# Kernel tuning notes

Hardware: AMD Instinct MI355X
Metric: run time of the kernel (lower is better)

The kernel has to match this reference:

```python
import jax, jax.numpy as jnp
import numpy as np

B, H, W, C = 8, 64, 64, 256
C8 = C // 8  # query/key channels


def setup_inputs() -> dict:
    key = jax.random.key(0)
    ks = jax.random.split(key, 8)
    s = 0.02  # init scale for weights
    return {
        "x": jax.random.normal(ks[0], (B, H, W, C), dtype=jnp.float32),
        "Wq": jax.random.normal(ks[1], (C, C8), dtype=jnp.float32) * s,
        "bq": jnp.zeros((C8,), dtype=jnp.float32),
        "Wk": jax.random.normal(ks[2], (C, C8), dtype=jnp.float32) * s,
        "bk": jnp.zeros((C8,), dtype=jnp.float32),
        "Wv": jax.random.normal(ks[3], (C, C), dtype=jnp.float32) * s,
        "bv": jnp.zeros((C,), dtype=jnp.float32),
        "gamma": jnp.full((1,), 0.5, dtype=jnp.float32),
    }


def reference(x, Wq, bq, Wk, bk, Wv, bv, gamma):
    Bn, Hn, Wn, Cn = x.shape
    N = Hn * Wn
    xf = x.reshape(Bn, N, Cn)            # flatten spatial dims: [B, N, C]
    # 1x1 convs == per-pixel dense projections over channels
    q = xf @ Wq + bq                     # [B, N, C//8]
    k = xf @ Wk + bk                     # [B, N, C//8]
    v = xf @ Wv + bv                     # [B, N, C]
    # energy[b,i,j] = k_i . q_j  (matches tf.matmul(key, query, transpose_b=True))
    energy = jnp.einsum('bic,bjc->bij', k, q)   # [B, N, N]
    attn = jax.nn.softmax(energy, axis=-1)      # softmax over last axis
    # out_i = sum_j attn[i,j] * v_j  (intended SAGAN aggregation in NHWC layout)
    out = jnp.einsum('bij,bjc->bic', attn, v)   # [B, N, C]
    out = out.reshape(Bn, Hn, Wn, Cn)
    return gamma * out + x
```

## Files before the change

kernel.cpp:

```cpp
#include <hip/hip_runtime.h>

typedef __attribute__((ext_vector_type(8))) short short8;
typedef __attribute__((ext_vector_type(4))) float f32x4;
typedef __attribute__((ext_vector_type(16))) float f32x16;
typedef __attribute__((ext_vector_type(2))) unsigned int u32x2;
typedef __attribute__((ext_vector_type(4))) unsigned int u32x4;
typedef unsigned short u16;
typedef unsigned int u32;

#define MFMA16(a, b, c) __builtin_amdgcn_mfma_f32_16x16x32_bf16((a), (b), (c), 0, 0, 0)
#define MFMA32(a, b, c) __builtin_amdgcn_mfma_f32_32x32x16_bf16((a), (b), (c), 0, 0, 0)

#define BAR_VMEM() asm volatile("s_waitcnt vmcnt(0) lgkmcnt(0)\ns_barrier" ::: "memory")
#define BAR_LDS()  asm volatile("s_waitcnt lgkmcnt(0)\ns_barrier" ::: "memory")

#define BATCH 8
#define NTOK 4096
#define CDIM 256
#define CQK 32
#define LOG2E 1.4426950408889634f

__device__ __forceinline__ u16 f2bf(float f) {
  u32 u = __float_as_uint(f);
  return (u16)((u + 0x7FFFu + ((u >> 16) & 1u)) >> 16);
}
__device__ __forceinline__ u32 pack2(float a, float b) {
  const u32 ua = __float_as_uint(a) + 0x8000u;
  const u32 ub = __float_as_uint(b) + 0x8000u;
#if __has_builtin(__builtin_amdgcn_perm)
  return __builtin_amdgcn_perm(ub, ua, 0x07060302u);
#else
  return (ua >> 16) | (ub & 0xFFFF0000u);
#endif
}
__device__ __forceinline__ float fexp2(float x) {
#if __has_builtin(__builtin_amdgcn_exp2f)
  return __builtin_amdgcn_exp2f(x);
#else
  return exp2f(x);
#endif
}
__device__ __forceinline__ void gl_lds16(const u16* g, u16* l) {
  __builtin_amdgcn_global_load_lds(
      (const __attribute__((address_space(1))) unsigned int*)(g),
      (__attribute__((address_space(3))) unsigned int*)(l), 16, 0, 0);
}

__global__ void k_prep(const float* __restrict__ Wq, const float* __restrict__ bq,
                       const float* __restrict__ Wk, const float* __restrict__ bk,
                       const float* __restrict__ Wv, const float* __restrict__ bv,
                       u16* __restrict__ wtf, float* __restrict__ bias) {
  const int f = blockIdx.x;
  const int L = threadIdx.x;
  const int ct = f >> 3, ks = f & 7;
  const int o = ct * 16 + (L & 15);
  const int ch = ks * 32 + (L >> 4) * 8;
  short8 v8;
#pragma unroll
  for (int jj = 0; jj < 8; jj++) {
    const int c = ch + jj;
    float v;
    if (o < 32)       v = Wq[c * CQK + o];
    else if (o < 64)  v = Wk[c * CQK + (o - 32)];
    else              v = Wv[c * CDIM + (o - 64)];
    v8[jj] = (short)f2bf(v);
  }
  *(short8*)(wtf + (size_t)f * 512 + L * 8) = v8;
  if (f == 0) {
    for (int i = L; i < 320; i += 64) {
      if (i < 32)      bias[i] = bq[i];
      else if (i < 64) bias[i] = bk[i - 32];
      else             bias[i] = bv[i - 64];
    }
  }
}

__global__ __launch_bounds__(256, 2) void k_proj(
    const float* __restrict__ x, const u16* __restrict__ wtf,
    const float* __restrict__ bias,
    u16* __restrict__ q_ws, u16* __restrict__ k_ws, u16* __restrict__ vt_ws) {
  __shared__ u16 x_lds[64 * 264];
  __shared__ u16 vt_t[64 * 72];
  const int m0 = blockIdx.x * 64;
  const int tid = threadIdx.x;
  const int w = tid >> 6, L = tid & 63;
  const int lr = L & 15, q4 = L >> 4;

  short8 wfA[5], wfB[5];
#pragma unroll
  for (int j = 0; j < 5; j++)
    wfA[j] = *(const short8*)(wtf + ((size_t)((j * 4 + w) * 8 + 0)) * 512 + L * 8);

#pragma unroll
  for (int ii = 0; ii < 8; ii++) {
    const int e = (tid + 256 * ii) * 8;
    const int row = e >> 8, col = e & 255;
    const float* src = x + (size_t)(m0 + row) * CDIM + col;
    f32x4 a = *(const f32x4*)src;
    f32x4 b4 = *(const f32x4*)(src + 4);
    u32x4 pk;
    pk[0] = pack2(a[0], a[1]);
    pk[1] = pack2(a[2], a[3]);
    pk[2] = pack2(b4[0], b4[1]);
    pk[3] = pack2(b4[2], b4[3]);
    *(u32x4*)&x_lds[row * 264 + col] = pk;
  }
  __syncthreads();

  f32x4 acc[4][5];
#pragma unroll
  for (int rg = 0; rg < 4; rg++)
#pragma unroll
    for (int j = 0; j < 5; j++) acc[rg][j] = (f32x4){0.f, 0.f, 0.f, 0.f};

#pragma unroll
  for (int ks = 0; ks < 8; ks++) {
    if (ks < 7) {
#pragma unroll
      for (int j = 0; j < 5; j++) {
        short8 v = *(const short8*)(wtf +
            ((size_t)((j * 4 + w) * 8 + ks + 1)) * 512 + L * 8);
        if (ks & 1) wfA[j] = v; else wfB[j] = v;
      }
    }
#pragma unroll
    for (int rg = 0; rg < 4; rg++) {
      short8 a = *(const short8*)&x_lds[(rg * 16 + lr) * 264 + ks * 32 + q4 * 8];
#pragma unroll
      for (int j = 0; j < 5; j++)
        acc[rg][j] = MFMA16(a, (ks & 1) ? wfB[j] : wfA[j], acc[rg][j]);
    }
  }

  {
    const float bb = bias[w * 16 + lr];
#pragma unroll
    for (int rg = 0; rg < 4; rg++)
#pragma unroll
      for (int r = 0; r < 4; r++) {
        const int row = m0 + rg * 16 + q4 * 4 + r;
        float v = acc[rg][0][r] + bb;
        if (w < 2) q_ws[(size_t)row * CQK + w * 16 + lr] = f2bf(v);
        else       k_ws[(size_t)row * CQK + (w - 2) * 16 + lr] = f2bf(v * LOG2E);
      }
  }
  const int b = m0 >> 12, nloc = m0 & 4095;
  const int rb2 = ((lr >> 3) & 1) << 2;
  const int c_l = w * 16 + lr;
#pragma unroll
  for (int cg = 0; cg < 4; cg++) {
    __syncthreads();
    const int j = cg + 1;
    const float bb = bias[(4 + cg * 4 + w) * 16 + lr];
#pragma unroll
    for (int rg = 0; rg < 4; rg++) {
      const int n_base = (rg * 16 + q4 * 4) ^ rb2;
      u32x2 pk;
      pk[0] = pack2(acc[rg][j][0] + bb, acc[rg][j][1] + bb);
      pk[1] = pack2(acc[rg][j][2] + bb, acc[rg][j][3] + bb);
      *(u32x2*)&vt_t[c_l * 72 + n_base] = pk;
    }
    __syncthreads();
#pragma unroll
    for (int i = 0; i < 2; i++) {
      const int gch = tid + 256 * i;
      const int cl2 = gch >> 3, jc = gch & 7;
      short8 v = *(const short8*)&vt_t[cl2 * 72 + jc * 8];
      *(short8*)(vt_ws + ((size_t)(b * CDIM + cg * 64 + cl2)) * NTOK + nloc + jc * 8) = v;
    }
  }
}

__global__ __launch_bounds__(256, 2) void k_attn(
    const float* __restrict__ x, const u16* __restrict__ q_ws,
    const u16* __restrict__ k_ws, const u16* __restrict__ vt_ws,
    const float* __restrict__ gamma, float* __restrict__ out) {
  __shared__ u16 vt_lds[2][256 * 64];
  __shared__ u16 p_lds[2][64 * 64];

  const int bid = blockIdx.x;
  const int b = bid & 7;
  const int it = bid >> 3;
  const int i0 = it * 64;
  const int tid = threadIdx.x;
  const int w = tid >> 6, L = tid & 63;
  const int lr = L & 15, q4 = L >> 4;
  const int L31 = L & 31, Lhi = L >> 5, L7 = L & 7;

  const short8 a_k = *(const short8*)(k_ws +
      ((size_t)(b * NTOK + i0 + w * 16 + lr)) * CQK + q4 * 8);

  const int cl_base = tid >> 3;
  const int jc_sw = (tid & 7) ^ (cl_base & 7);
  const u16* vt_g = vt_ws + ((size_t)(b * CDIM + cl_base)) * NTOK + jc_sw * 8;
  const u16* q_base = q_ws + (size_t)b * NTOK * CQK;

  f32x16 o_acc[2][2];
#pragma unroll
  for (int ih = 0; ih < 2; ih++)
#pragma unroll
    for (int ct2 = 0; ct2 < 2; ct2++)
#pragma unroll
      for (int e = 0; e < 16; e++) o_acc[ih][ct2][e] = 0.f;
  float lsum = 0.f;

  const int pw_off = (w * 16 + lr) * 64 + (((q4 & 1) ^ ((lr >> 3) & 1)) << 2);
  const int q4h = q4 >> 1;
  u16* const pl0 = &p_lds[0][0];
  u16* const pl1 = &p_lds[1][0];

#define EXPW(SV, T, PW)                                                          \
  do {                                                                           \
    const float p0 = fexp2((SV)[0]);                                             \
    const float p1 = fexp2((SV)[1]);                                             \
    const float p2 = fexp2((SV)[2]);                                             \
    const float p3 = fexp2((SV)[3]);                                             \
    lsum += (p0 + p1) + (p2 + p3);                                               \
    u32x2 pk;                                                                    \
    pk[0] = pack2(p0, p1);                                                       \
    pk[1] = pack2(p2, p3);                                                       \
    *(u32x2*)((PW) + (((2 * (T) + q4h) ^ (lr & 7)) * 8)) = pk;                   \
  } while (0)

  short8 bqA[4], bqB[4];
#pragma unroll
  for (int t = 0; t < 4; t++)
    bqA[t] = *(const short8*)(q_base + (size_t)(t * 16 + lr) * CQK + q4 * 8);
#pragma unroll
  for (int ii = 0; ii < 8; ii++)
    gl_lds16(vt_g + (size_t)(ii * 32) * NTOK, &vt_lds[0][ii * 2048 + w * 512]);
  {
    f32x4 s0 = MFMA16(bqA[0], a_k, ((f32x4){0.f, 0.f, 0.f, 0.f}));
    f32x4 s1 = MFMA16(bqA[1], a_k, ((f32x4){0.f, 0.f, 0.f, 0.f}));
    f32x4 s2 = MFMA16(bqA[2], a_k, ((f32x4){0.f, 0.f, 0.f, 0.f}));
    f32x4 s3 = MFMA16(bqA[3], a_k, ((f32x4){0.f, 0.f, 0.f, 0.f}));
    u16* pwn = pl0 + pw_off;
    EXPW(s0, 0, pwn);
    EXPW(s1, 1, pwn);
    EXPW(s2, 2, pwn);
    EXPW(s3, 3, pwn);
  }
#pragma unroll
  for (int t = 0; t < 4; t++)
    bqB[t] = *(const short8*)(q_base + (size_t)(64 + t * 16 + lr) * CQK + q4 * 8);

#define ATTN_ITER(JT, PL_CUR, PL_NXT, VB_CUR, VB_NXT, BQN, BQF, DO_Q)            \
  do {                                                                           \
    const int j0 = (JT) * 64;                                                    \
    BAR_VMEM();    \
    _Pragma("unroll")                                                            \
    for (int ii = 0; ii < 8; ii++)                                               \
      gl_lds16(vt_g + (size_t)(ii * 32) * NTOK + (j0 + 64),                      \
               &VB_NXT[ii * 2048 + w * 512]);                                    \
       \
    f32x4 s0 = MFMA16(BQN[0], a_k, ((f32x4){0.f, 0.f, 0.f, 0.f}));               \
    f32x4 s1 = MFMA16(BQN[1], a_k, ((f32x4){0.f, 0.f, 0.f, 0.f}));               \
    f32x4 s2 = MFMA16(BQN[2], a_k, ((f32x4){0.f, 0.f, 0.f, 0.f}));               \
    f32x4 s3 = MFMA16(BQN[3], a_k, ((f32x4){0.f, 0.f, 0.f, 0.f}));               \
    u16* pwn = (PL_NXT) + pw_off;                                                \
            \
    _Pragma("unroll")                                                            \
    for (int ks = 0; ks < 4; ks++) {                                             \
      const int slot = (((ks * 2 + Lhi) ^ L7)) * 8;                              \
      short8 a_p0 = *(const short8*)((PL_CUR) + L31 * 64 + slot);                \
      short8 a_p1 = *(const short8*)((PL_CUR) + (32 + L31) * 64 + slot);         \
      _Pragma("unroll")                                                          \
      for (int ct2 = 0; ct2 < 2; ct2++) {                                        \
        const int cl = w * 64 + ct2 * 32 + L31;                                  \
        short8 b_v = *(const short8*)((VB_CUR) + cl * 64 + slot);                \
        o_acc[0][ct2] = MFMA32(a_p0, b_v, o_acc[0][ct2]);                        \
        o_acc[1][ct2] = MFMA32(a_p1, b_v, o_acc[1][ct2]);                        \
      }                                                                          \
      if (ks == 0) EXPW(s0, 0, pwn);                                             \
      if (ks == 1) EXPW(s1, 1, pwn);                                             \
      if (ks == 2) EXPW(s2, 2, pwn);                                             \
      if (ks == 3) EXPW(s3, 3, pwn);                                             \
    }                                                                            \
    if (DO_Q) {                                                                  \
      _Pragma("unroll")                                                          \
      for (int t = 0; t < 4; t++)                                                \
        BQF[t] = *(const short8*)(q_base +                                       \
                 (size_t)(j0 + 128 + t * 16 + lr) * CQK + q4 * 8);               \
    }                                                                            \
  } while (0)

  for (int jt2 = 0; jt2 < 62; jt2 += 2) {
    ATTN_ITER(jt2,     pl0, pl1, (&vt_lds[0][0]), (&vt_lds[1][0]), bqB, bqA, 1);
    ATTN_ITER(jt2 + 1, pl1, pl0, (&vt_lds[1][0]), (&vt_lds[0][0]), bqA, bqB, 1);
  }
  ATTN_ITER(62, pl0, pl1, (&vt_lds[0][0]), (&vt_lds[1][0]), bqB, bqA, 0);
#undef ATTN_ITER

  BAR_VMEM();
#pragma unroll
  for (int ks = 0; ks < 4; ks++) {
    const int slot = (((ks * 2 + Lhi) ^ L7)) * 8;
    short8 a_p0 = *(const short8*)(pl1 + L31 * 64 + slot);
    short8 a_p1 = *(const short8*)(pl1 + (32 + L31) * 64 + slot);
#pragma unroll
    for (int ct2 = 0; ct2 < 2; ct2++) {
      const int cl = w * 64 + ct2 * 32 + L31;
      short8 b_v = *(const short8*)(&vt_lds[1][0] + cl * 64 + slot);
      o_acc[0][ct2] = MFMA32(a_p0, b_v, o_acc[0][ct2]);
      o_acc[1][ct2] = MFMA32(a_p1, b_v, o_acc[1][ct2]);
    }
  }
#undef EXPW

  float s2 = lsum;
  s2 += __shfl_xor(s2, 16);
  s2 += __shfl_xor(s2, 32);
  const float rl = 1.0f / s2;
  BAR_LDS();
  float* lp = (float*)pl0;
  if (q4 == 0) lp[w * 16 + lr] = rl;
  BAR_LDS();

  float linv2[2][16];
#pragma unroll
  for (int ih = 0; ih < 2; ih++)
#pragma unroll
    for (int rg = 0; rg < 16; rg++)
      linv2[ih][rg] = lp[ih * 32 + (rg & 3) + 8 * (rg >> 2) + 4 * Lhi];

  const float g = gamma[0];
#pragma unroll
  for (int ih = 0; ih < 2; ih++)
#pragma unroll
    for (int ct2 = 0; ct2 < 2; ct2++) {
      const int c = w * 64 + ct2 * 32 + L31;
#pragma unroll
      for (int rg = 0; rg < 16; rg++) {
        const int i = i0 + ih * 32 + (rg & 3) + 8 * (rg >> 2) + 4 * Lhi;
        const size_t idx = ((size_t)(b * NTOK + i)) * CDIM + c;
        out[idx] = g * (o_acc[ih][ct2][rg] * linv2[ih][rg]) + x[idx];
      }
    }
}

extern "C" void kernel_launch(void* const* d_in, const int* in_sizes, int n_in,
                              void* d_out, int out_size, void* d_ws, size_t ws_size,
                              hipStream_t stream) {
  const float* x  = (const float*)d_in[0];
  const float* Wq = (const float*)d_in[1];
  const float* bq = (const float*)d_in[2];
  const float* Wk = (const float*)d_in[3];
  const float* bk = (const float*)d_in[4];
  const float* Wv = (const float*)d_in[5];
  const float* bv = (const float*)d_in[6];
  const float* gamma = (const float*)d_in[7];
  float* out = (float*)d_out;

  char* ws = (char*)d_ws;
  u16* q_ws  = (u16*)(ws);
  u16* k_ws  = (u16*)(ws + (2u << 20));
  u16* vt_ws = (u16*)(ws + (4u << 20));
  u16* wtf   = (u16*)(ws + (20u << 20));
  float* bias = (float*)(ws + (20u << 20) + (256u << 10));

  k_prep<<<160, 64, 0, stream>>>(Wq, bq, Wk, bk, Wv, bv, wtf, bias);
  k_proj<<<512, 256, 0, stream>>>(x, wtf, bias, q_ws, k_ws, vt_ws);
  k_attn<<<512, 256, 0, stream>>>(x, q_ws, k_ws, vt_ws, gamma, out);
}
```

Measured before the change: 195.3 us.

## Store V in MFMA fragment order and stream it directly into registers

```diff
diff --git a/kernel.cpp b/kernel.cpp
--- a/kernel.cpp
+++ b/kernel.cpp
@@ -39,11 +39,6 @@
 #else
   return exp2f(x);
 #endif
-}
-__device__ __forceinline__ void gl_lds16(const u16* g, u16* l) {
-  __builtin_amdgcn_global_load_lds(
-      (const __attribute__((address_space(1))) unsigned int*)(g),
-      (__attribute__((address_space(3))) unsigned int*)(l), 16, 0, 0);
 }
 
 __global__ void k_prep(const float* __restrict__ Wq, const float* __restrict__ bq,
@@ -144,7 +139,7 @@
         else       k_ws[(size_t)row * CQK + (w - 2) * 16 + lr] = f2bf(v * LOG2E);
       }
   }
-  const int b = m0 >> 12, nloc = m0 & 4095;
+  const int b = m0 >> 12, nt = (m0 & 4095) >> 6;
   const int rb2 = ((lr >> 3) & 1) << 2;
   const int c_l = w * 16 + lr;
 #pragma unroll
@@ -164,9 +159,13 @@
 #pragma unroll
     for (int i = 0; i < 2; i++) {
       const int gch = tid + 256 * i;
-      const int cl2 = gch >> 3, jc = gch & 7;
-      short8 v = *(const short8*)&vt_t[cl2 * 72 + jc * 8];
-      *(short8*)(vt_ws + ((size_t)(b * CDIM + cg * 64 + cl2)) * NTOK + nloc + jc * 8) = v;
+      const int fi = gch >> 6;
+      const int lane = gch & 63;
+      const int ks2 = fi >> 1, ct2 = fi & 1;
+      short8 v = *(const short8*)&vt_t[(ct2 * 32 + (lane & 31)) * 72 +
+                                       (ks2 * 2 + (lane >> 5)) * 8];
+      *(short8*)(vt_ws +
+          ((((size_t)(b * 64 + nt) * 4 + cg) * 8 + fi) * 512) + lane * 8) = v;
     }
   }
 }
@@ -175,7 +174,6 @@
     const float* __restrict__ x, const u16* __restrict__ q_ws,
     const u16* __restrict__ k_ws, const u16* __restrict__ vt_ws,
     const float* __restrict__ gamma, float* __restrict__ out) {
-  __shared__ u16 vt_lds[2][256 * 64];
   __shared__ u16 p_lds[2][64 * 64];
 
   const int bid = blockIdx.x;
@@ -190,9 +188,7 @@
   const short8 a_k = *(const short8*)(k_ws +
       ((size_t)(b * NTOK + i0 + w * 16 + lr)) * CQK + q4 * 8);
 
-  const int cl_base = tid >> 3;
-  const int jc_sw = (tid & 7) ^ (cl_base & 7);
-  const u16* vt_g = vt_ws + ((size_t)(b * CDIM + cl_base)) * NTOK + jc_sw * 8;
+  const u16* vg = vt_ws + (((size_t)b * 256 + w) * 8) * 512 + (size_t)L * 8;
   const u16* q_base = q_ws + (size_t)b * NTOK * CQK;
 
   f32x16 o_acc[2][2];
@@ -223,12 +219,13 @@
   } while (0)
 
   short8 bqA[4], bqB[4];
+  short8 vV[8];
 #pragma unroll
   for (int t = 0; t < 4; t++)
     bqA[t] = *(const short8*)(q_base + (size_t)(t * 16 + lr) * CQK + q4 * 8);
 #pragma unroll
-  for (int ii = 0; ii < 8; ii++)
-    gl_lds16(vt_g + (size_t)(ii * 32) * NTOK, &vt_lds[0][ii * 2048 + w * 512]);
+  for (int fi = 0; fi < 8; fi++)
+    vV[fi] = *(const short8*)(vg + (size_t)fi * 512);
   {
     f32x4 s0 = MFMA16(bqA[0], a_k, ((f32x4){0.f, 0.f, 0.f, 0.f}));
     f32x4 s1 = MFMA16(bqA[1], a_k, ((f32x4){0.f, 0.f, 0.f, 0.f}));
@@ -244,66 +241,57 @@
   for (int t = 0; t < 4; t++)
     bqB[t] = *(const short8*)(q_base + (size_t)(64 + t * 16 + lr) * CQK + q4 * 8);
 
-#define ATTN_ITER(JT, PL_CUR, PL_NXT, VB_CUR, VB_NXT, BQN, BQF, DO_Q)            \
+#define ATTN_ITER(JT, PL_CUR, PL_NXT, BQN, BQF, DO_Q)                            \
   do {                                                                           \
-    const int j0 = (JT) * 64;                                                    \
-    BAR_VMEM();    \
-    _Pragma("unroll")                                                            \
-    for (int ii = 0; ii < 8; ii++)                                               \
-      gl_lds16(vt_g + (size_t)(ii * 32) * NTOK + (j0 + 64),                      \
-               &VB_NXT[ii * 2048 + w * 512]);                                    \
-       \
+    BAR_LDS();          \
     f32x4 s0 = MFMA16(BQN[0], a_k, ((f32x4){0.f, 0.f, 0.f, 0.f}));               \
     f32x4 s1 = MFMA16(BQN[1], a_k, ((f32x4){0.f, 0.f, 0.f, 0.f}));               \
     f32x4 s2 = MFMA16(BQN[2], a_k, ((f32x4){0.f, 0.f, 0.f, 0.f}));               \
     f32x4 s3 = MFMA16(BQN[3], a_k, ((f32x4){0.f, 0.f, 0.f, 0.f}));               \
+    if (DO_Q) {                                                                  \
+      _Pragma("unroll")                                                          \
+      for (int t = 0; t < 4; t++)                                                \
+        BQF[t] = *(const short8*)(q_base +                                       \
+                 (size_t)((JT) * 64 + 128 + t * 16 + lr) * CQK + q4 * 8);        \
+    }                                                                            \
     u16* pwn = (PL_NXT) + pw_off;                                                \
-            \
     _Pragma("unroll")                                                            \
     for (int ks = 0; ks < 4; ks++) {                                             \
       const int slot = (((ks * 2 + Lhi) ^ L7)) * 8;                              \
       short8 a_p0 = *(const short8*)((PL_CUR) + L31 * 64 + slot);                \
       short8 a_p1 = *(const short8*)((PL_CUR) + (32 + L31) * 64 + slot);         \
-      _Pragma("unroll")                                                          \
-      for (int ct2 = 0; ct2 < 2; ct2++) {                                        \
-        const int cl = w * 64 + ct2 * 32 + L31;                                  \
-        short8 b_v = *(const short8*)((VB_CUR) + cl * 64 + slot);                \
-        o_acc[0][ct2] = MFMA32(a_p0, b_v, o_acc[0][ct2]);                        \
-        o_acc[1][ct2] = MFMA32(a_p1, b_v, o_acc[1][ct2]);                        \
-      }                                                                          \
+      o_acc[0][0] = MFMA32(a_p0, vV[ks * 2 + 0], o_acc[0][0]);                   \
+      o_acc[1][0] = MFMA32(a_p1, vV[ks * 2 + 0], o_acc[1][0]);                   \
+      o_acc[0][1] = MFMA32(a_p0, vV[ks * 2 + 1], o_acc[0][1]);                   \
+      o_acc[1][1] = MFMA32(a_p1, vV[ks * 2 + 1], o_acc[1][1]);                   \
+      vV[ks * 2 + 0] = *(const short8*)(vg +                                     \
+          (size_t)((JT) + 1) * 16384 + (ks * 2 + 0) * 512);                      \
+      vV[ks * 2 + 1] = *(const short8*)(vg +                                     \
+          (size_t)((JT) + 1) * 16384 + (ks * 2 + 1) * 512);                      \
       if (ks == 0) EXPW(s0, 0, pwn);                                             \
       if (ks == 1) EXPW(s1, 1, pwn);                                             \
       if (ks == 2) EXPW(s2, 2, pwn);                                             \
       if (ks == 3) EXPW(s3, 3, pwn);                                             \
     }                                                                            \
-    if (DO_Q) {                                                                  \
-      _Pragma("unroll")                                                          \
-      for (int t = 0; t < 4; t++)                                                \
-        BQF[t] = *(const short8*)(q_base +                                       \
-                 (size_t)(j0 + 128 + t * 16 + lr) * CQK + q4 * 8);               \
-    }                                                                            \
   } while (0)
 
   for (int jt2 = 0; jt2 < 62; jt2 += 2) {
-    ATTN_ITER(jt2,     pl0, pl1, (&vt_lds[0][0]), (&vt_lds[1][0]), bqB, bqA, 1);
-    ATTN_ITER(jt2 + 1, pl1, pl0, (&vt_lds[1][0]), (&vt_lds[0][0]), bqA, bqB, 1);
-  }
-  ATTN_ITER(62, pl0, pl1, (&vt_lds[0][0]), (&vt_lds[1][0]), bqB, bqA, 0);
+    ATTN_ITER(jt2,     pl0, pl1, bqB, bqA, 1);
+    ATTN_ITER(jt2 + 1, pl1, pl0, bqA, bqB, 1);
+  }
+  ATTN_ITER(62, pl0, pl1, bqB, bqA, 0);
 #undef ATTN_ITER
 
-  BAR_VMEM();
+  BAR_LDS();
 #pragma unroll
   for (int ks = 0; ks < 4; ks++) {
     const int slot = (((ks * 2 + Lhi) ^ L7)) * 8;
     short8 a_p0 = *(const short8*)(pl1 + L31 * 64 + slot);
     short8 a_p1 = *(const short8*)(pl1 + (32 + L31) * 64 + slot);
-#pragma unroll
-    for (int ct2 = 0; ct2 < 2; ct2++) {
-      const int cl = w * 64 + ct2 * 32 + L31;
-      short8 b_v = *(const short8*)(&vt_lds[1][0] + cl * 64 + slot);
-      o_acc[0][ct2] = MFMA32(a_p0, b_v, o_acc[0][ct2]);
-      o_acc[1][ct2] = MFMA32(a_p1, b_v, o_acc[1][ct2]);
-    }
+    o_acc[0][0] = MFMA32(a_p0, vV[ks * 2 + 0], o_acc[0][0]);
+    o_acc[1][0] = MFMA32(a_p1, vV[ks * 2 + 0], o_acc[1][0]);
+    o_acc[0][1] = MFMA32(a_p0, vV[ks * 2 + 1], o_acc[0][1]);
+    o_acc[1][1] = MFMA32(a_p1, vV[ks * 2 + 1], o_acc[1][1]);
   }
 #undef EXPW
 
```

Result: faster. 185.1 us (-5.3%).
